# Optimization experiments

Measured on AMD Instinct MI355X. Metric: run time of the kernel, lower is better.

Reference implementation:

```python
import jax, jax.numpy as jnp
import numpy as np

B, S, D = 4, 4096, 64

def setup_inputs() -> dict:
    key = jax.random.key(0)
    kq, kk, kv = jax.random.split(key, 3)
    q = jax.random.normal(kq, (B, S, D), dtype=jnp.float32)
    k = jax.random.normal(kk, (B, S, D), dtype=jnp.float32)
    v = jax.random.normal(kv, (B, S, D), dtype=jnp.float32)
    return {"q": q, "k": k, "v": v}

def reference(q, k, v):
    d_k = k.shape[-1]
    # scores: [B, S, S]
    scores = jnp.einsum('bqd,bkd->bqk', q, k) / jnp.sqrt(jnp.asarray(d_k, q.dtype))
    s = scores.shape[-1]
    # causal mask: disallow j > i (strict upper triangle)
    causal = jnp.tril(jnp.ones((scores.shape[-2], s), dtype=bool))
    scores = jnp.where(causal, scores, jnp.asarray(-jnp.inf, scores.dtype))
    norm_scores = jax.nn.softmax(scores, axis=-1)
    return jnp.einsum('bqk,bkd->bqd', norm_scores, v)
```

## Files before the change

kernel.cpp:

```cpp
#include <hip/hip_runtime.h>

#define B_ 4
#define S_ 4096
#define D_ 64

typedef __attribute__((ext_vector_type(8))) short short8;
typedef __attribute__((ext_vector_type(4))) float f32x4;
typedef __attribute__((ext_vector_type(16))) float f32x16;
typedef __attribute__((ext_vector_type(4))) int int4v;
typedef __attribute__((ext_vector_type(2))) unsigned uint2v;
typedef unsigned short u16;

__device__ __forceinline__ unsigned pack_bf2(float a, float b) {
  unsigned ua = __float_as_uint(a) + 0x8000u;
  unsigned ub = __float_as_uint(b) + 0x8000u;
  return __builtin_amdgcn_perm(ub, ua, 0x07060302);
}

__device__ __forceinline__ uint2v permswap(unsigned a, unsigned b) {
#if __has_builtin(__builtin_amdgcn_permlane32_swap)
  return __builtin_amdgcn_permlane32_swap(a, b, false, false);
#else
  int h = (threadIdx.x >> 5) & 1;
  unsigned ta = __shfl_xor(a, 32);
  unsigned tb = __shfl_xor(b, 32);
  uint2v r;
  r[0] = h ? tb : a;
  r[1] = h ? b : ta;
  return r;
#endif
}

__global__ __launch_bounds__(256) void cvt_all_k(const float* __restrict__ q,
                                                 const float* __restrict__ k,
                                                 const float* __restrict__ v,
                                                 u16* __restrict__ wsQ,
                                                 u16* __restrict__ wsK,
                                                 u16* __restrict__ wsV) {
  int blk = blockIdx.x;
  if (blk < 1024) {
    const float* src = (blk < 512) ? q : k;
    u16* dst = (blk < 512) ? wsQ : wsK;
    float scale = (blk < 512) ? 0.18033688011112042f : 1.0f;
    int t = ((blk & 511) << 8) + threadIdx.x;
    const f32x4* s4 = (const f32x4*)src;
    f32x4 a = s4[2 * t], b = s4[2 * t + 1];
    int4v r;
    r[0] = (int)pack_bf2(a[0] * scale, a[1] * scale);
    r[1] = (int)pack_bf2(a[2] * scale, a[3] * scale);
    r[2] = (int)pack_bf2(b[0] * scale, b[1] * scale);
    r[3] = (int)pack_bf2(b[2] * scale, b[3] * scale);
    *(int4v*)(dst + 8 * (long)t) = r;
  } else {
    int t = ((blk - 1024) << 8) + threadIdx.x;
    int lane = t & 63;
    int J  = (t >> 6) & 3;
    int dt = (t >> 8) & 1;
    int ck = (t >> 9) & 63;
    int b  = t >> 15;
    int row = ck * 64 + J * 16 + (lane >> 5) * 8;
    int col = dt * 32 + (lane & 31);
    const float* src = v + ((long)(b * S_ + row)) * D_ + col;
    float e[8];
#pragma unroll
    for (int i = 0; i < 8; i++) e[i] = src[(long)i * D_];
    int4v r;
    r[0] = (int)pack_bf2(e[0], e[1]);
    r[1] = (int)pack_bf2(e[2], e[3]);
    r[2] = (int)pack_bf2(e[4], e[5]);
    r[3] = (int)pack_bf2(e[6], e[7]);
    *(int4v*)(wsV + 8 * (long)t) = r;
  }
}

#define MFMA32(a, bb, cc) __builtin_amdgcn_mfma_f32_32x32x16_bf16((a), (bb), (cc), 0, 0, 0)

__global__ __launch_bounds__(512, 2) void attn_k(const u16* __restrict__ wsQ,
                                                 const u16* __restrict__ wsK,
                                                 const u16* __restrict__ wsV,
                                                 float* __restrict__ out) {
  int bid = blockIdx.x;
  int b   = bid & 3;
  int g32 = 127 - (bid >> 2);
  int tid = threadIdx.x;
  int w = tid >> 6, lane = tid & 63, c2 = lane & 31, h = lane >> 5;
  int cmax = g32 >> 1;
  int q0 = g32 * 32;

  __shared__ float sMem[8][2176];
  __shared__ float sML[8][32];

  float* W = &sMem[w][0];

  short8 qf[4];
#pragma unroll
  for (int kk = 0; kk < 4; kk++)
    qf[kk] = *(const short8*)(wsQ + ((long)(b * S_ + q0 + c2)) * D_ + kk * 16 + h * 8);

  f32x16 o0, o1;
#pragma unroll
  for (int r = 0; r < 16; r++) { o0[r] = 0.f; o1[r] = 0.f; }
  float lp = 0.f;

  for (int ck = w; ck <= cmax; ck += 8) {
    const u16* kp = wsK + ((long)(b * S_ + ck * 64 + c2)) * D_ + h * 8;
    short8 kf[2][4];
#pragma unroll
    for (int jt = 0; jt < 2; jt++)
#pragma unroll
      for (int kk = 0; kk < 4; kk++)
        kf[jt][kk] = *(const short8*)(kp + jt * 32 * D_ + kk * 16);
    const u16* vp = wsV + ((long)(b * 64 + ck)) * 4096 + (long)lane * 8;
    short8 vf[2][4];
#pragma unroll
    for (int dt = 0; dt < 2; dt++)
#pragma unroll
      for (int J = 0; J < 4; J++)
        vf[dt][J] = *(const short8*)(vp + (dt * 4 + J) * 512);

    f32x16 s[2];
#pragma unroll
    for (int r = 0; r < 16; r++) { s[0][r] = 0.f; s[1][r] = 0.f; }
#pragma unroll
    for (int kk = 0; kk < 4; kk++) {
      s[0] = MFMA32(kf[0][kk], qf[kk], s[0]);
      s[1] = MFMA32(kf[1][kk], qf[kk], s[1]);
    }

    if (ck == cmax) {
      int dq = 32 * (g32 & 1) + c2;
#pragma unroll
      for (int r = 0; r < 16; r++) {
        int row = (r & 3) + 8 * (r >> 2) + 4 * h;
        if (row      > dq) s[0][r] = -1e30f;
        if (row + 32 > dq) s[1][r] = -1e30f;
      }
    }

    float sum = 0.f;
#pragma unroll
    for (int r = 0; r < 16; r++) {
      s[0][r] = exp2f(s[0][r]); sum += s[0][r];
      s[1][r] = exp2f(s[1][r]); sum += s[1][r];
    }
    lp += sum;

    short8 p[4];
#pragma unroll
    for (int jt = 0; jt < 2; jt++) {
      unsigned D[8];
#pragma unroll
      for (int g = 0; g < 4; g++) {
        D[2 * g]     = pack_bf2(s[jt][4 * g],     s[jt][4 * g + 1]);
        D[2 * g + 1] = pack_bf2(s[jt][4 * g + 2], s[jt][4 * g + 3]);
      }
#pragma unroll
      for (int e = 0; e < 2; e++) {
        uint2v r0 = permswap(D[4 * e],     D[4 * e + 2]);
        uint2v r1 = permswap(D[4 * e + 1], D[4 * e + 3]);
        int4v pw;
        pw[0] = (int)r0[0]; pw[1] = (int)r1[0];
        pw[2] = (int)r0[1]; pw[3] = (int)r1[1];
        p[2 * jt + e] = __builtin_bit_cast(short8, pw);
      }
    }

#pragma unroll
    for (int J = 0; J < 4; J++) {
      o0 = MFMA32(vf[0][J], p[J], o0);
      o1 = MFMA32(vf[1][J], p[J], o1);
    }
  }

  lp += __shfl_xor(lp, 32);
  if (h == 0) sML[w][c2] = lp;
#pragma unroll
  for (int dt = 0; dt < 2; dt++)
#pragma unroll
    for (int grp = 0; grp < 4; grp++) {
      f32x4 t4;
      const f32x16& ov = dt ? o1 : o0;
      t4[0] = ov[4 * grp]; t4[1] = ov[4 * grp + 1];
      t4[2] = ov[4 * grp + 2]; t4[3] = ov[4 * grp + 3];
      *(f32x4*)&W[c2 * 68 + 32 * dt + 8 * grp + 4 * h] = t4;
    }
  __syncthreads();

  int q = tid >> 4, d4 = tid & 15;
  float L = 0.f;
  f32x4 acc = {0.f, 0.f, 0.f, 0.f};
#pragma unroll
  for (int w2 = 0; w2 < 8; w2++) {
    L += sML[w2][q];
    f32x4 pv = *(f32x4*)&sMem[w2][q * 68 + d4 * 4];
#pragma unroll
    for (int i = 0; i < 4; i++) acc[i] += pv[i];
  }
  float inv = 1.f / L;
  f32x4 r;
#pragma unroll
  for (int i = 0; i < 4; i++) r[i] = acc[i] * inv;
  *(f32x4*)(out + ((long)(b * S_ + q0 + q)) * D_ + d4 * 4) = r;
}

extern "C" void kernel_launch(void* const* d_in, const int* in_sizes, int n_in,
                              void* d_out, int out_size, void* d_ws, size_t ws_size,
                              hipStream_t stream) {
  const float* q = (const float*)d_in[0];
  const float* k = (const float*)d_in[1];
  const float* v = (const float*)d_in[2];
  float* out = (float*)d_out;

  u16* wsQ = (u16*)d_ws;
  u16* wsK = wsQ + (long)B_ * S_ * D_;
  u16* wsV = wsK + (long)B_ * S_ * D_;

  cvt_all_k<<<1536, 256, 0, stream>>>(q, k, v, wsQ, wsK, wsV);
  attn_k<<<512, 512, 0, stream>>>(wsQ, wsK, wsV, out);
}
```

Before: 91.85 us.

## Double-buffer K/V register fragments and use native exp2 with split sums

Restructures the per-wave chunk loop into a two-stage software pipeline that prefetches the next chunk's K and V fragments into a second register buffer while the current chunk's MFMAs and softmax run. The aim is to hide global-load latency behind compute. It also switches exp2f to the hardware exp2 builtin and splits the row-sum into four partial accumulators to shorten the dependency chain. The extra fragment buffers raise register pressure under the 512-thread, 2-blocks-per-CU launch bound, which could cause spills or lower occupancy.

```diff
diff --git a/kernel.cpp b/kernel.cpp
--- a/kernel.cpp
+++ b/kernel.cpp
@@ -15,6 +15,14 @@
   unsigned ua = __float_as_uint(a) + 0x8000u;
   unsigned ub = __float_as_uint(b) + 0x8000u;
   return __builtin_amdgcn_perm(ub, ua, 0x07060302);
+}
+
+__device__ __forceinline__ float fexp2(float x) {
+#if __has_builtin(__builtin_amdgcn_exp2f)
+  return __builtin_amdgcn_exp2f(x);
+#else
+  return exp2f(x);
+#endif
 }
 
 __device__ __forceinline__ uint2v permswap(unsigned a, unsigned b) {
@@ -86,6 +94,7 @@
   int w = tid >> 6, lane = tid & 63, c2 = lane & 31, h = lane >> 5;
   int cmax = g32 >> 1;
   int q0 = g32 * 32;
+  int dq = 32 * (g32 & 1) + c2;
 
   __shared__ float sMem[8][2176];
   __shared__ float sML[8][32];
@@ -102,22 +111,25 @@
   for (int r = 0; r < 16; r++) { o0[r] = 0.f; o1[r] = 0.f; }
   float lp = 0.f;
 
-  for (int ck = w; ck <= cmax; ck += 8) {
-    const u16* kp = wsK + ((long)(b * S_ + ck * 64 + c2)) * D_ + h * 8;
-    short8 kf[2][4];
+  const u16* kbase = wsK + ((long)(b * S_ + c2)) * D_ + h * 8;
+  const u16* vbase = wsV + ((long)(b * 64)) * 4096 + (long)lane * 8;
+
+  auto loadKV = [&](short8 (&kf)[2][4], short8 (&vf)[2][4], int ck) {
+    const u16* kp = kbase + (long)ck * 64 * D_;
 #pragma unroll
     for (int jt = 0; jt < 2; jt++)
 #pragma unroll
       for (int kk = 0; kk < 4; kk++)
         kf[jt][kk] = *(const short8*)(kp + jt * 32 * D_ + kk * 16);
-    const u16* vp = wsV + ((long)(b * 64 + ck)) * 4096 + (long)lane * 8;
-    short8 vf[2][4];
+    const u16* vp = vbase + (long)ck * 4096;
 #pragma unroll
     for (int dt = 0; dt < 2; dt++)
 #pragma unroll
       for (int J = 0; J < 4; J++)
         vf[dt][J] = *(const short8*)(vp + (dt * 4 + J) * 512);
-
+  };
+
+  auto compute = [&](short8 (&kf)[2][4], short8 (&vf)[2][4], int ck) {
     f32x16 s[2];
 #pragma unroll
     for (int r = 0; r < 16; r++) { s[0][r] = 0.f; s[1][r] = 0.f; }
@@ -128,7 +140,6 @@
     }
 
     if (ck == cmax) {
-      int dq = 32 * (g32 & 1) + c2;
 #pragma unroll
       for (int r = 0; r < 16; r++) {
         int row = (r & 3) + 8 * (r >> 2) + 4 * h;
@@ -137,27 +148,36 @@
       }
     }
 
-    float sum = 0.f;
-#pragma unroll
-    for (int r = 0; r < 16; r++) {
-      s[0][r] = exp2f(s[0][r]); sum += s[0][r];
-      s[1][r] = exp2f(s[1][r]); sum += s[1][r];
-    }
-    lp += sum;
+    float su0 = 0.f, su1 = 0.f, su2 = 0.f, su3 = 0.f;
+#pragma unroll
+    for (int r = 0; r < 4; r++) {
+      s[0][r]      = fexp2(s[0][r]);      su0 += s[0][r];
+      s[0][r + 4]  = fexp2(s[0][r + 4]);  su1 += s[0][r + 4];
+      s[0][r + 8]  = fexp2(s[0][r + 8]);  su2 += s[0][r + 8];
+      s[0][r + 12] = fexp2(s[0][r + 12]); su3 += s[0][r + 12];
+    }
+#pragma unroll
+    for (int r = 0; r < 4; r++) {
+      s[1][r]      = fexp2(s[1][r]);      su0 += s[1][r];
+      s[1][r + 4]  = fexp2(s[1][r + 4]);  su1 += s[1][r + 4];
+      s[1][r + 8]  = fexp2(s[1][r + 8]);  su2 += s[1][r + 8];
+      s[1][r + 12] = fexp2(s[1][r + 12]); su3 += s[1][r + 12];
+    }
+    lp += (su0 + su1) + (su2 + su3);
 
     short8 p[4];
 #pragma unroll
     for (int jt = 0; jt < 2; jt++) {
-      unsigned D[8];
+      unsigned Dw[8];
 #pragma unroll
       for (int g = 0; g < 4; g++) {
-        D[2 * g]     = pack_bf2(s[jt][4 * g],     s[jt][4 * g + 1]);
-        D[2 * g + 1] = pack_bf2(s[jt][4 * g + 2], s[jt][4 * g + 3]);
+        Dw[2 * g]     = pack_bf2(s[jt][4 * g],     s[jt][4 * g + 1]);
+        Dw[2 * g + 1] = pack_bf2(s[jt][4 * g + 2], s[jt][4 * g + 3]);
       }
 #pragma unroll
       for (int e = 0; e < 2; e++) {
-        uint2v r0 = permswap(D[4 * e],     D[4 * e + 2]);
-        uint2v r1 = permswap(D[4 * e + 1], D[4 * e + 3]);
+        uint2v r0 = permswap(Dw[4 * e],     Dw[4 * e + 2]);
+        uint2v r1 = permswap(Dw[4 * e + 1], Dw[4 * e + 3]);
         int4v pw;
         pw[0] = (int)r0[0]; pw[1] = (int)r1[0];
         pw[2] = (int)r0[1]; pw[3] = (int)r1[1];
@@ -170,6 +190,18 @@
       o0 = MFMA32(vf[0][J], p[J], o0);
       o1 = MFMA32(vf[1][J], p[J], o1);
     }
+  };
+
+  short8 kfA[2][4], vfA[2][4], kfB[2][4], vfB[2][4];
+  int ck0 = w;
+  if (ck0 <= cmax) loadKV(kfA, vfA, ck0);
+  for (int ck = ck0; ck <= cmax; ck += 16) {
+    int ckB = ck + 8;
+    if (ckB <= cmax) loadKV(kfB, vfB, ckB);
+    compute(kfA, vfA, ck);
+    int ckA2 = ck + 16;
+    if (ckA2 <= cmax) loadKV(kfA, vfA, ckA2);
+    if (ckB <= cmax) compute(kfB, vfB, ckB);
   }
 
   lp += __shfl_xor(lp, 32);
```

Result: no change. 92.58 us (+0.8%).
